# Performance work log

Hardware: AMD Instinct MI355X
Metric: run time of the kernel (lower is better)

## Reference

```python
import jax, jax.numpy as jnp
import numpy as np

DMODEL = 512
NUM_HEADS = 8
HEAD_DIM = DMODEL // NUM_HEADS
ATTN_LEN = 5
BATCH = 4
SEQ = 4096


def kv_roll(t, layer, shift):
    # t: [B, h_sub, T, 1, hd]; replicates tf.pad + tf.roll + concat + slice
    T = t.shape[2]
    dil = 2 ** layer
    p = dil * (ATTN_LEN // 2)
    tp = jnp.pad(t, ((0, 0), (0, 0), (p, p), (0, 0), (0, 0)))
    # circular rolls, concat along the singleton window axis -> [B,h,T+2p,ATTN_LEN,hd]
    rolled = jnp.concatenate(
        [jnp.roll(tp, -i * dil, axis=2) for i in range(shift, ATTN_LEN + shift)],
        axis=3,
    )
    return rolled[:, :, :T]


def setup_inputs() -> dict:
    key = jax.random.key(0)
    ks = jax.random.split(key, 8)
    inputs = jax.random.normal(ks[0], (BATCH, SEQ, DMODEL), dtype=jnp.float32)
    Wq = jax.random.normal(ks[1], (DMODEL, DMODEL), dtype=jnp.float32) * 0.02
    bq = jnp.zeros((DMODEL,), dtype=jnp.float32)
    Wk = jax.random.normal(ks[2], (DMODEL, DMODEL), dtype=jnp.float32) * 0.02
    bk = jnp.zeros((DMODEL,), dtype=jnp.float32)
    Wv = jax.random.normal(ks[3], (DMODEL, DMODEL), dtype=jnp.float32) * 0.02
    bv = jnp.zeros((DMODEL,), dtype=jnp.float32)
    Er = jax.random.normal(ks[4], (NUM_HEADS, HEAD_DIM, ATTN_LEN), dtype=jnp.float32) * 0.05
    return {"inputs": inputs, "Wq": Wq, "bq": bq, "Wk": Wk, "bk": bk,
            "Wv": Wv, "bv": bv, "Er": Er, "layer": 1}


def reference(inputs, Wq, bq, Wk, bk, Wv, bv, Er, layer):
    B, T, D = inputs.shape
    # projections -> [B, H, T, 1, hd]
    def proj(W, b):
        x = inputs @ W + b
        x = x.reshape(B, T, NUM_HEADS, 1, HEAD_DIM)
        return jnp.transpose(x, (0, 2, 1, 3, 4))
    q = proj(Wq, bq)
    k = proj(Wk, bk)
    v = proj(Wv, bv)

    def build_windows(t):
        # per-head-group shifts: heads 0-3 shift 0, head 4 shift -2, head 5 -1, head 6 +1, head 7 +2
        return jnp.concatenate((
            kv_roll(t[:, 0:4], layer, 0),
            kv_roll(t[:, 4:5], layer, -2),
            kv_roll(t[:, 5:6], layer, -1),
            kv_roll(t[:, 6:7], layer, 1),
            kv_roll(t[:, 7:8], layer, 2),
        ), axis=1)  # [B, H, T, ATTN_LEN, hd]

    kw = build_windows(k)
    vw = build_windows(v)

    # qk: [B, H, T, 1, ATTN_LEN]
    qk = jnp.einsum('bhtqd,bhtwd->bhtqw', q, kw)
    # relative positional bias: q @ Er -> [B, H, T, 1, ATTN_LEN]
    qEr = jnp.einsum('bhtqd,hdw->bhtqw', q, Er)
    scale = jnp.sqrt(jnp.float32(HEAD_DIM)).astype(inputs.dtype)
    logits = (qk + qEr) / scale
    mask = (qk == 0).astype(logits.dtype)
    attn = jax.nn.softmax(logits + mask * -10000.0, axis=-1)
    # out: [B, H, T, 1, hd]
    out = jnp.einsum('bhtqw,bhtwd->bhtqd', attn, vw)
    out = jnp.transpose(out[:, :, :, 0, :], (0, 2, 1, 3)).reshape(B, T, D)
    return out, attn
```

## Files before the change

### kernel.cpp

```cpp
#include <hip/hip_runtime.h>
#include <stdint.h>

#define B_ 4
#define T_ 4096
#define D_ 512
#define H_ 8
#define HD_ 64
#define W_ 5
#define M_ (B_*T_)
#define N_ (3*D_)

typedef __attribute__((ext_vector_type(8))) short short8;
typedef __attribute__((ext_vector_type(4))) float floatx4;

__device__ __forceinline__ unsigned short f2bf(float f) {
    unsigned int u = __builtin_bit_cast(unsigned int, f);
    u += 0x7fffu + ((u >> 16) & 1u);
    return (unsigned short)(u >> 16);
}
__device__ __forceinline__ float bf2f(unsigned short s) {
    unsigned int u = ((unsigned int)s) << 16;
    return __builtin_bit_cast(float, u);
}
__device__ __forceinline__ void load8bf(const unsigned short* p, float* f) {
    uint4 d = *(const uint4*)p;
    f[0] = bf2f((unsigned short)(d.x & 0xffffu));
    f[1] = bf2f((unsigned short)(d.x >> 16));
    f[2] = bf2f((unsigned short)(d.y & 0xffffu));
    f[3] = bf2f((unsigned short)(d.y >> 16));
    f[4] = bf2f((unsigned short)(d.z & 0xffffu));
    f[5] = bf2f((unsigned short)(d.z >> 16));
    f[6] = bf2f((unsigned short)(d.w & 0xffffu));
    f[7] = bf2f((unsigned short)(d.w >> 16));
}

__device__ __forceinline__ void async16(const unsigned short* g, unsigned short* l) {
    __builtin_amdgcn_global_load_lds(
        (const __attribute__((address_space(1))) unsigned int*)g,
        (__attribute__((address_space(3))) unsigned int*)l, 16, 0, 0);
}

__global__ __launch_bounds__(256) void convert_x(const float* __restrict__ x,
                                                 unsigned short* __restrict__ xb) {
    int i = blockIdx.x * 256 + threadIdx.x;
    const float4* x4 = (const float4*)x;
    float4 a = x4[2*i], b = x4[2*i + 1];
    uint4 o;
    o.x = (unsigned)f2bf(a.x) | ((unsigned)f2bf(a.y) << 16);
    o.y = (unsigned)f2bf(a.z) | ((unsigned)f2bf(a.w) << 16);
    o.z = (unsigned)f2bf(b.x) | ((unsigned)f2bf(b.y) << 16);
    o.w = (unsigned)f2bf(b.z) | ((unsigned)f2bf(b.w) << 16);
    ((uint4*)xb)[i] = o;
}

__global__ __launch_bounds__(256) void convert_w(const float* __restrict__ Wq,
                                                 const float* __restrict__ Wk,
                                                 const float* __restrict__ Wv,
                                                 unsigned short* __restrict__ Wt) {
    int tid = blockIdx.x * 256 + threadIdx.x;
    int n  = tid % N_;
    int kc = tid / N_;
    int proj = n >> 9, c = n & 511;
    const float* Wsrc = (proj == 0) ? Wq : ((proj == 1) ? Wk : Wv);
    unsigned short us[8];
#pragma unroll
    for (int j = 0; j < 8; j++)
        us[j] = f2bf(Wsrc[(size_t)(kc*8 + j) * D_ + c]);
    uint4 o;
    o.x = (unsigned)us[0] | ((unsigned)us[1] << 16);
    o.y = (unsigned)us[2] | ((unsigned)us[3] << 16);
    o.z = (unsigned)us[4] | ((unsigned)us[5] << 16);
    o.w = (unsigned)us[6] | ((unsigned)us[7] << 16);
    *(uint4*)(Wt + (size_t)n * D_ + kc*8) = o;
}

__global__ __launch_bounds__(256) void gemm_qkv(
    const unsigned short* __restrict__ Xb,
    const unsigned short* __restrict__ Wt,
    const float* __restrict__ bq, const float* __restrict__ bk2,
    const float* __restrict__ bv,
    unsigned short* __restrict__ Cb)
{
    __shared__ unsigned short As[128 * 32];
    __shared__ unsigned short Bs[128 * 32];
    const int tid = threadIdx.x;
    const int m0 = blockIdx.y * 128;
    const int n0 = blockIdx.x * 128;
    const int wave = tid >> 6, lane = tid & 63;
    const int wm = (wave >> 1) << 6, wn = (wave & 1) << 6;
    const int qd = lane >> 4, r16 = lane & 15;

    const int arow = wave * 32 + (lane >> 2);
    const int acol = (lane & 3) * 8;
    const unsigned short* ag = Xb + (size_t)(m0 + arow) * D_ + acol;
    const unsigned short* bg = Wt + (size_t)(n0 + arow) * D_ + acol;
    unsigned short* al = As + (wave * 32) * 32;
    unsigned short* bl = Bs + (wave * 32) * 32;

    floatx4 acc[4][4] = {};

    for (int kc = 0; kc < D_; kc += 32) {
        async16(ag + kc,         al);
        async16(ag + 16*D_ + kc, al + 16*32);
        async16(bg + kc,         bl);
        async16(bg + 16*D_ + kc, bl + 16*32);
        __syncthreads();

        short8 af[4], bf[4];
#pragma unroll
        for (int mi = 0; mi < 4; mi++)
            af[mi] = __builtin_bit_cast(short8,
                *(const uint4*)(As + (wm + mi*16 + r16)*32 + qd*8));
#pragma unroll
        for (int ni = 0; ni < 4; ni++)
            bf[ni] = __builtin_bit_cast(short8,
                *(const uint4*)(Bs + (wn + ni*16 + r16)*32 + qd*8));
#pragma unroll
        for (int mi = 0; mi < 4; mi++)
#pragma unroll
            for (int ni = 0; ni < 4; ni++)
                acc[mi][ni] = __builtin_amdgcn_mfma_f32_16x16x32_bf16(
                    af[mi], bf[ni], acc[mi][ni], 0, 0, 0);
        __syncthreads();
    }

#pragma unroll
    for (int ni = 0; ni < 4; ni++) {
        int col = n0 + wn + ni*16 + r16;
        float bias = (col < 512) ? bq[col] : ((col < 1024) ? bk2[col - 512] : bv[col - 1024]);
#pragma unroll
        for (int mi = 0; mi < 4; mi++) {
#pragma unroll
            for (int r = 0; r < 4; r++) {
                int row = m0 + wm + mi*16 + qd*4 + r;
                Cb[(size_t)row * N_ + col] = f2bf(acc[mi][ni][r] + bias);
            }
        }
    }
}

__global__ __launch_bounds__(256) void attn_kernel(
    const unsigned short* __restrict__ Cb,
    const float* __restrict__ Er,
    const int* __restrict__ layer_p,
    float* __restrict__ out,
    float* __restrict__ attn_out)
{
    __shared__ float sEr[HD_ * W_];
    const int bx = blockIdx.x;
    const int bh = bx >> 7;
    const int chunk = bx & 127;
    const int b = bh >> 3, h = bh & 7;
    const int tid = threadIdx.x;
    const int g = tid >> 3, c8 = tid & 7;
    const int t = chunk * 32 + g;

    for (int i = tid; i < HD_ * W_; i += 256)
        sEr[i] = Er[h * HD_ * W_ + i];
    __syncthreads();

    const int dil = 1 << layer_p[0];
    const int sh = (h < 4) ? 0 : (h == 4 ? -2 : (h == 5 ? -1 : (h == 6 ? 1 : 2)));

    int pos[W_]; bool val[W_];
#pragma unroll
    for (int w = 0; w < W_; w++) {
        pos[w] = t + (sh + w - 2) * dil;
        val[w] = (pos[w] >= 0) && (pos[w] < T_);
    }

    const size_t bT = (size_t)b * T_;
    const unsigned short* qp    = Cb + (bT + t) * N_ + h * HD_ + c8 * 8;
    const unsigned short* kbase = Cb + bT * N_ + 512  + h * HD_ + c8 * 8;
    const unsigned short* vbase = Cb + bT * N_ + 1024 + h * HD_ + c8 * 8;

    float qf[8]; load8bf(qp, qf);

    float s[W_];
#pragma unroll
    for (int w = 0; w < W_; w++) {
        float a = 0.f;
        if (val[w]) {
            float kf[8]; load8bf(kbase + (size_t)pos[w] * N_, kf);
#pragma unroll
            for (int j = 0; j < 8; j++) a = fmaf(qf[j], kf[j], a);
        }
#pragma unroll
        for (int j = 0; j < 8; j++)
            a = fmaf(qf[j], sEr[(c8*8 + j) * W_ + w], a);
        s[w] = a;
    }
#pragma unroll
    for (int off = 4; off > 0; off >>= 1)
#pragma unroll
        for (int w = 0; w < W_; w++)
            s[w] += __shfl_xor(s[w], off, 8);

    float logit[W_], mx = -1e30f;
#pragma unroll
    for (int w = 0; w < W_; w++) {
        logit[w] = val[w] ? s[w] * 0.125f : -1e30f;
        mx = fmaxf(mx, logit[w]);
    }
    float p[W_], ssum = 0.f;
#pragma unroll
    for (int w = 0; w < W_; w++) {
        p[w] = val[w] ? __expf(logit[w] - mx) : 0.f;
        ssum += p[w];
    }
    const float inv = 1.f / ssum;
    float aw[W_];
#pragma unroll
    for (int w = 0; w < W_; w++) aw[w] = p[w] * inv;

    if (c8 < W_)
        attn_out[((size_t)(b * H_ + h) * T_ + t) * W_ + c8] = aw[c8];

    float of[8] = {0,0,0,0,0,0,0,0};
#pragma unroll
    for (int w = 0; w < W_; w++) {
        if (val[w]) {
            float vf[8]; load8bf(vbase + (size_t)pos[w] * N_, vf);
#pragma unroll
            for (int j = 0; j < 8; j++) of[j] = fmaf(aw[w], vf[j], of[j]);
        }
    }
    float* orow = out + (bT + t) * D_ + h * HD_ + c8 * 8;
    *(float4*)(orow)     = make_float4(of[0], of[1], of[2], of[3]);
    *(float4*)(orow + 4) = make_float4(of[4], of[5], of[6], of[7]);
}

extern "C" void kernel_launch(void* const* d_in, const int* in_sizes, int n_in,
                              void* d_out, int out_size, void* d_ws, size_t ws_size,
                              hipStream_t stream) {
    const float* x   = (const float*)d_in[0];
    const float* Wq  = (const float*)d_in[1];
    const float* bq  = (const float*)d_in[2];
    const float* Wk  = (const float*)d_in[3];
    const float* bk  = (const float*)d_in[4];
    const float* Wv  = (const float*)d_in[5];
    const float* bv  = (const float*)d_in[6];
    const float* Er  = (const float*)d_in[7];
    const int* layer = (const int*)d_in[8];

    char* ws = (char*)d_ws;
    unsigned short* Xb = (unsigned short*)ws;
    unsigned short* Wt = (unsigned short*)(ws + (size_t)16*1024*1024);
    unsigned short* Cb = (unsigned short*)(ws + (size_t)18*1024*1024);

    float* out  = (float*)d_out;
    float* attn = out + (size_t)B_ * T_ * D_;

    convert_x<<<(M_ * D_ / 8) / 256, 256, 0, stream>>>(x, Xb);
    convert_w<<<(N_ * (D_ / 8)) / 256, 256, 0, stream>>>(Wq, Wk, Wv, Wt);
    dim3 g(N_ / 128, M_ / 128);
    gemm_qkv<<<g, 256, 0, stream>>>(Xb, Wt, bq, bk, bv, Cb);
    attn_kernel<<<(B_ * H_ * T_ * 8) / 256, 256, 0, stream>>>(Cb, Er, layer, out, attn);
}
```

Measured before the change: 161.6 us.

## Fuse QKV projection GEMM with windowed attention per head tile

Replaces the separate QKV GEMM and attention kernels with one kernel. Each block computes Q, K and V for one head over 128 tokens plus a 16-row halo on each side, writes them as bf16 into LDS, then runs the 5-tap windowed softmax attention directly from LDS. The weights are reordered per head so each block's 192 output columns are contiguous. This removes the global round trip of the bf16 QKV intermediate, at the cost of recomputing the halo rows (160 rows per 128 tokens), larger per-block LDS use that limits occupancy, and a halo that only covers dilation offsets up to 16.

```diff
diff --git a/kernel.cpp b/kernel.cpp
--- a/kernel.cpp
+++ b/kernel.cpp
@@ -8,7 +8,10 @@
 #define HD_ 64
 #define W_ 5
 #define M_ (B_*T_)
-#define N_ (3*D_)
+#define TM 160
+#define TN 192
+#define HALO 16
+#define LSTR 72
 
 typedef __attribute__((ext_vector_type(8))) short short8;
 typedef __attribute__((ext_vector_type(4))) float floatx4;
@@ -53,15 +56,17 @@
     ((uint4*)xb)[i] = o;
 }
 
-__global__ __launch_bounds__(256) void convert_w(const float* __restrict__ Wq,
-                                                 const float* __restrict__ Wk,
-                                                 const float* __restrict__ Wv,
-                                                 unsigned short* __restrict__ Wt) {
+__global__ __launch_bounds__(256) void convert_w2(const float* __restrict__ Wq,
+                                                  const float* __restrict__ Wk,
+                                                  const float* __restrict__ Wv,
+                                                  unsigned short* __restrict__ Wt2) {
     int tid = blockIdx.x * 256 + threadIdx.x;
-    int n  = tid % N_;
-    int kc = tid / N_;
-    int proj = n >> 9, c = n & 511;
-    const float* Wsrc = (proj == 0) ? Wq : ((proj == 1) ? Wk : Wv);
+    int np = tid % 1536;
+    int kc = tid / 1536;
+    int h = np / 192, n192 = np % 192;
+    int sel = n192 >> 6, ch = n192 & 63;
+    int c = h * 64 + ch;
+    const float* Wsrc = (sel == 0) ? Wq : ((sel == 1) ? Wk : Wv);
     unsigned short us[8];
 #pragma unroll
     for (int j = 0; j < 8; j++)
@@ -71,163 +76,166 @@
     o.y = (unsigned)us[2] | ((unsigned)us[3] << 16);
     o.z = (unsigned)us[4] | ((unsigned)us[5] << 16);
     o.w = (unsigned)us[6] | ((unsigned)us[7] << 16);
-    *(uint4*)(Wt + (size_t)n * D_ + kc*8) = o;
-}
-
-__global__ __launch_bounds__(256) void gemm_qkv(
+    *(uint4*)(Wt2 + (size_t)np * D_ + kc*8) = o;
+}
+
+__global__ __launch_bounds__(256) void fused_qkv_attn(
     const unsigned short* __restrict__ Xb,
-    const unsigned short* __restrict__ Wt,
+    const unsigned short* __restrict__ Wt2,
     const float* __restrict__ bq, const float* __restrict__ bk2,
-    const float* __restrict__ bv,
-    unsigned short* __restrict__ Cb)
-{
-    __shared__ unsigned short As[128 * 32];
-    __shared__ unsigned short Bs[128 * 32];
-    const int tid = threadIdx.x;
-    const int m0 = blockIdx.y * 128;
-    const int n0 = blockIdx.x * 128;
-    const int wave = tid >> 6, lane = tid & 63;
-    const int wm = (wave >> 1) << 6, wn = (wave & 1) << 6;
-    const int qd = lane >> 4, r16 = lane & 15;
-
-    const int arow = wave * 32 + (lane >> 2);
-    const int acol = (lane & 3) * 8;
-    const unsigned short* ag = Xb + (size_t)(m0 + arow) * D_ + acol;
-    const unsigned short* bg = Wt + (size_t)(n0 + arow) * D_ + acol;
-    unsigned short* al = As + (wave * 32) * 32;
-    unsigned short* bl = Bs + (wave * 32) * 32;
-
-    floatx4 acc[4][4] = {};
-
-    for (int kc = 0; kc < D_; kc += 32) {
-        async16(ag + kc,         al);
-        async16(ag + 16*D_ + kc, al + 16*32);
-        async16(bg + kc,         bl);
-        async16(bg + 16*D_ + kc, bl + 16*32);
-        __syncthreads();
-
-        short8 af[4], bf[4];
-#pragma unroll
-        for (int mi = 0; mi < 4; mi++)
-            af[mi] = __builtin_bit_cast(short8,
-                *(const uint4*)(As + (wm + mi*16 + r16)*32 + qd*8));
-#pragma unroll
-        for (int ni = 0; ni < 4; ni++)
-            bf[ni] = __builtin_bit_cast(short8,
-                *(const uint4*)(Bs + (wn + ni*16 + r16)*32 + qd*8));
-#pragma unroll
-        for (int mi = 0; mi < 4; mi++)
-#pragma unroll
-            for (int ni = 0; ni < 4; ni++)
-                acc[mi][ni] = __builtin_amdgcn_mfma_f32_16x16x32_bf16(
-                    af[mi], bf[ni], acc[mi][ni], 0, 0, 0);
-        __syncthreads();
-    }
-
-#pragma unroll
-    for (int ni = 0; ni < 4; ni++) {
-        int col = n0 + wn + ni*16 + r16;
-        float bias = (col < 512) ? bq[col] : ((col < 1024) ? bk2[col - 512] : bv[col - 1024]);
-#pragma unroll
-        for (int mi = 0; mi < 4; mi++) {
-#pragma unroll
-            for (int r = 0; r < 4; r++) {
-                int row = m0 + wm + mi*16 + qd*4 + r;
-                Cb[(size_t)row * N_ + col] = f2bf(acc[mi][ni][r] + bias);
-            }
-        }
-    }
-}
-
-__global__ __launch_bounds__(256) void attn_kernel(
-    const unsigned short* __restrict__ Cb,
-    const float* __restrict__ Er,
+    const float* __restrict__ bv, const float* __restrict__ Er,
     const int* __restrict__ layer_p,
     float* __restrict__ out,
     float* __restrict__ attn_out)
 {
+    __shared__ unsigned short SH[3 * TM * LSTR];
     __shared__ float sEr[HD_ * W_];
-    const int bx = blockIdx.x;
-    const int bh = bx >> 7;
-    const int chunk = bx & 127;
-    const int b = bh >> 3, h = bh & 7;
+    unsigned short* As = SH;
+    unsigned short* Bs = SH + TM * 32;
+    unsigned short* Qs = SH;
+    unsigned short* Ks = SH + TM * LSTR;
+    unsigned short* Vs = SH + 2 * TM * LSTR;
+
     const int tid = threadIdx.x;
-    const int g = tid >> 3, c8 = tid & 7;
-    const int t = chunk * 32 + g;
+    const int wave = tid >> 6, lane = tid & 63;
+    const int tile = blockIdx.x >> 3, h = blockIdx.x & 7;
+    const int b = tile >> 5;
+    const int t0 = (tile & 31) * 128;
+    const long m0g = (long)b * T_ + t0;
 
     for (int i = tid; i < HD_ * W_; i += 256)
         sEr[i] = Er[h * HD_ * W_ + i];
+
+    const unsigned short* gsrc[6];
+    unsigned short* ldst[6];
+#pragma unroll
+    for (int j = 0; j < 6; j++) {
+        int q = wave + j * 4;
+        if (q < 22) {
+            if (q < 10) {
+                long grow = m0g - HALO + q*16 + (lane >> 2);
+                grow = grow < 0 ? 0 : (grow >= M_ ? M_ - 1 : grow);
+                gsrc[j] = Xb + grow * D_ + (lane & 3) * 8;
+                ldst[j] = As + q * 512;
+            } else {
+                int q2 = q - 10;
+                gsrc[j] = Wt2 + ((size_t)h*192 + q2*16 + (lane >> 2)) * D_ + (lane & 3) * 8;
+                ldst[j] = Bs + q2 * 512;
+            }
+        }
+    }
+
+    const int wm = (wave >> 1) * 80, wn = (wave & 1) * 96;
+    const int qd = lane >> 4, r16 = lane & 15;
+    floatx4 acc[5][6] = {};
+
+    for (int kc = 0; kc < D_; kc += 32) {
+#pragma unroll
+        for (int j = 0; j < 6; j++)
+            if (wave + j * 4 < 22)
+                async16(gsrc[j] + kc, ldst[j]);
+        __syncthreads();
+        short8 af[5], bf[6];
+#pragma unroll
+        for (int mi = 0; mi < 5; mi++)
+            af[mi] = __builtin_bit_cast(short8,
+                *(const uint4*)(As + (wm + mi*16 + r16)*32 + qd*8));
+#pragma unroll
+        for (int ni = 0; ni < 6; ni++)
+            bf[ni] = __builtin_bit_cast(short8,
+                *(const uint4*)(Bs + (wn + ni*16 + r16)*32 + qd*8));
+#pragma unroll
+        for (int mi = 0; mi < 5; mi++)
+#pragma unroll
+            for (int ni = 0; ni < 6; ni++)
+                acc[mi][ni] = __builtin_amdgcn_mfma_f32_16x16x32_bf16(
+                    af[mi], bf[ni], acc[mi][ni], 0, 0, 0);
+        __syncthreads();
+    }
+
+#pragma unroll
+    for (int ni = 0; ni < 6; ni++) {
+        int n192 = wn + ni * 16 + r16;
+        int sel = n192 >> 6;
+        int ch = n192 & 63;
+        float bias = (sel == 0) ? bq[h*64 + ch]
+                   : (sel == 1) ? bk2[h*64 + ch] : bv[h*64 + ch];
+        unsigned short* tb = (sel == 0) ? Qs : (sel == 1) ? Ks : Vs;
+#pragma unroll
+        for (int mi = 0; mi < 5; mi++)
+#pragma unroll
+            for (int r = 0; r < 4; r++) {
+                int l = wm + mi*16 + qd*4 + r;
+                tb[l * LSTR + ch] = f2bf(acc[mi][ni][r] + bias);
+            }
+    }
     __syncthreads();
 
     const int dil = 1 << layer_p[0];
     const int sh = (h < 4) ? 0 : (h == 4 ? -2 : (h == 5 ? -1 : (h == 6 ? 1 : 2)));
-
-    int pos[W_]; bool val[W_];
-#pragma unroll
-    for (int w = 0; w < W_; w++) {
-        pos[w] = t + (sh + w - 2) * dil;
-        val[w] = (pos[w] >= 0) && (pos[w] < T_);
-    }
-
-    const size_t bT = (size_t)b * T_;
-    const unsigned short* qp    = Cb + (bT + t) * N_ + h * HD_ + c8 * 8;
-    const unsigned short* kbase = Cb + bT * N_ + 512  + h * HD_ + c8 * 8;
-    const unsigned short* vbase = Cb + bT * N_ + 1024 + h * HD_ + c8 * 8;
-
-    float qf[8]; load8bf(qp, qf);
-
-    float s[W_];
-#pragma unroll
-    for (int w = 0; w < W_; w++) {
-        float a = 0.f;
-        if (val[w]) {
-            float kf[8]; load8bf(kbase + (size_t)pos[w] * N_, kf);
-#pragma unroll
-            for (int j = 0; j < 8; j++) a = fmaf(qf[j], kf[j], a);
-        }
-#pragma unroll
-        for (int j = 0; j < 8; j++)
-            a = fmaf(qf[j], sEr[(c8*8 + j) * W_ + w], a);
-        s[w] = a;
-    }
-#pragma unroll
-    for (int off = 4; off > 0; off >>= 1)
-#pragma unroll
-        for (int w = 0; w < W_; w++)
-            s[w] += __shfl_xor(s[w], off, 8);
-
-    float logit[W_], mx = -1e30f;
-#pragma unroll
-    for (int w = 0; w < W_; w++) {
-        logit[w] = val[w] ? s[w] * 0.125f : -1e30f;
-        mx = fmaxf(mx, logit[w]);
-    }
-    float p[W_], ssum = 0.f;
-#pragma unroll
-    for (int w = 0; w < W_; w++) {
-        p[w] = val[w] ? __expf(logit[w] - mx) : 0.f;
-        ssum += p[w];
-    }
-    const float inv = 1.f / ssum;
-    float aw[W_];
-#pragma unroll
-    for (int w = 0; w < W_; w++) aw[w] = p[w] * inv;
-
-    if (c8 < W_)
-        attn_out[((size_t)(b * H_ + h) * T_ + t) * W_ + c8] = aw[c8];
-
-    float of[8] = {0,0,0,0,0,0,0,0};
-#pragma unroll
-    for (int w = 0; w < W_; w++) {
-        if (val[w]) {
-            float vf[8]; load8bf(vbase + (size_t)pos[w] * N_, vf);
-#pragma unroll
-            for (int j = 0; j < 8; j++) of[j] = fmaf(aw[w], vf[j], of[j]);
-        }
-    }
-    float* orow = out + (bT + t) * D_ + h * HD_ + c8 * 8;
-    *(float4*)(orow)     = make_float4(of[0], of[1], of[2], of[3]);
-    *(float4*)(orow + 4) = make_float4(of[4], of[5], of[6], of[7]);
+    const int c8 = tid & 7, g32 = tid >> 3;
+
+#pragma unroll
+    for (int p = 0; p < 4; p++) {
+        int tl = g32 + p * 32;
+        int t = t0 + tl;
+        float qf[8]; load8bf(Qs + (tl + HALO) * LSTR + c8 * 8, qf);
+
+        int pos[W_]; bool val[W_]; float s[W_];
+#pragma unroll
+        for (int w = 0; w < W_; w++) {
+            pos[w] = t + (sh + w - 2) * dil;
+            val[w] = (pos[w] >= 0) && (pos[w] < T_);
+            float a = 0.f;
+            if (val[w]) {
+                float kf[8]; load8bf(Ks + (pos[w] - t0 + HALO) * LSTR + c8 * 8, kf);
+#pragma unroll
+                for (int j = 0; j < 8; j++) a = fmaf(qf[j], kf[j], a);
+            }
+#pragma unroll
+            for (int j = 0; j < 8; j++)
+                a = fmaf(qf[j], sEr[(c8*8 + j) * W_ + w], a);
+            s[w] = a;
+        }
+#pragma unroll
+        for (int off = 4; off > 0; off >>= 1)
+#pragma unroll
+            for (int w = 0; w < W_; w++)
+                s[w] += __shfl_xor(s[w], off, 8);
+
+        float logit[W_], mx = -1e30f;
+#pragma unroll
+        for (int w = 0; w < W_; w++) {
+            logit[w] = val[w] ? s[w] * 0.125f : -1e30f;
+            mx = fmaxf(mx, logit[w]);
+        }
+        float pw[W_], ssum = 0.f;
+#pragma unroll
+        for (int w = 0; w < W_; w++) {
+            pw[w] = val[w] ? __expf(logit[w] - mx) : 0.f;
+            ssum += pw[w];
+        }
+        const float inv = 1.f / ssum;
+        float aw[W_];
+#pragma unroll
+        for (int w = 0; w < W_; w++) aw[w] = pw[w] * inv;
+
+        if (c8 < W_)
+            attn_out[((size_t)(b * H_ + h) * T_ + t) * W_ + c8] = aw[c8];
+
+        float of[8] = {0,0,0,0,0,0,0,0};
+#pragma unroll
+        for (int w = 0; w < W_; w++) {
+            if (val[w]) {
+                float vf[8]; load8bf(Vs + (pos[w] - t0 + HALO) * LSTR + c8 * 8, vf);
+#pragma unroll
+                for (int j = 0; j < 8; j++) of[j] = fmaf(aw[w], vf[j], of[j]);
+            }
+        }
+        float* orow = out + ((size_t)b * T_ + t) * D_ + h * HD_ + c8 * 8;
+        *(float4*)(orow)     = make_float4(of[0], of[1], of[2], of[3]);
+        *(float4*)(orow + 4) = make_float4(of[4], of[5], of[6], of[7]);
+    }
 }
 
 extern "C" void kernel_launch(void* const* d_in, const int* in_sizes, int n_in,
@@ -244,16 +252,14 @@
     const int* layer = (const int*)d_in[8];
 
     char* ws = (char*)d_ws;
-    unsigned short* Xb = (unsigned short*)ws;
-    unsigned short* Wt = (unsigned short*)(ws + (size_t)16*1024*1024);
-    unsigned short* Cb = (unsigned short*)(ws + (size_t)18*1024*1024);
+    unsigned short* Xb  = (unsigned short*)ws;
+    unsigned short* Wt2 = (unsigned short*)(ws + (size_t)16*1024*1024);
 
     float* out  = (float*)d_out;
     float* attn = out + (size_t)B_ * T_ * D_;
 
     convert_x<<<(M_ * D_ / 8) / 256, 256, 0, stream>>>(x, Xb);
-    convert_w<<<(N_ * (D_ / 8)) / 256, 256, 0, stream>>>(Wq, Wk, Wv, Wt);
-    dim3 g(N_ / 128, M_ / 128);
-    gemm_qkv<<<g, 256, 0, stream>>>(Xb, Wt, bq, bk, bv, Cb);
-    attn_kernel<<<(B_ * H_ * T_ * 8) / 256, 256, 0, stream>>>(Cb, Er, layer, out, attn);
-}
+    convert_w2<<<(1536 * 64) / 256, 256, 0, stream>>>(Wq, Wk, Wv, Wt2);
+    fused_qkv_attn<<<(M_ / 128) * 8, 256, 0, stream>>>(Xb, Wt2, bq, bk, bv,
+                                                       Er, layer, out, attn);
+}
```

After: 198.8 us. 23.1% more time.
